# Performance work log

Hardware: AMD Instinct MI355X
Metric: run time of the kernel (lower is better)

Reference implementation:

```python
import jax, jax.numpy as jnp
import numpy as np

EPS = 1e-8  # matches torch.nn.functional.cosine_similarity default eps


def setup_inputs() -> dict:
    key = jax.random.key(0)
    k1, k2 = jax.random.split(key)
    B, C, L, D = 65536, 64, 64, 128
    x = jax.random.normal(k1, (B, D), dtype=jnp.float32)
    category_embeddings = jax.random.normal(k2, (C, L, D), dtype=jnp.float32)
    leaf_usage_counts = jnp.zeros((C, L), dtype=jnp.float32)
    return {
        "x": x,
        "category_embeddings": category_embeddings,
        "leaf_usage_counts": leaf_usage_counts,
    }


def reference(x, category_embeddings, leaf_usage_counts):
    # Cosine similarity: [B, C, L] without materializing the broadcast [B,C,L,D].
    x_norm = jnp.maximum(jnp.linalg.norm(x, axis=-1, keepdims=True), EPS)        # [B, 1]
    e_norm = jnp.maximum(jnp.linalg.norm(category_embeddings, axis=-1), EPS)     # [C, L]
    dots = jnp.einsum('bd,cld->bcl', x, category_embeddings)                     # [B, C, L]
    cosine_sim = dots / (x_norm[:, :, None] * e_norm[None, :, :])                # [B, C, L]

    # Training-path usage-count update (done under no_grad in torch):
    # per-category bincount of argmax leaf, scatter-added into the buffer.
    max_indices = jnp.argmax(cosine_sim, axis=2)                                 # [B, C] int
    C, L = leaf_usage_counts.shape
    cat_ids = jnp.broadcast_to(jnp.arange(C)[None, :], max_indices.shape)        # [B, C]
    leaf_counts = jnp.zeros((C, L), jnp.float32).at[cat_ids, max_indices].add(1.0)
    new_leaf_usage_counts = leaf_usage_counts + leaf_counts                      # [C, L]

    cosine_sim_max = jnp.max(cosine_sim, axis=2)                                 # [B, C]
    return cosine_sim_max, new_leaf_usage_counts
```

## Files before the change

kernel.cpp:

```cpp
#include <hip/hip_runtime.h>
#include <stdint.h>
#include <stddef.h>

#define D      128
#define NCATS  64
#define NLEAF  64
#define NC_BLK 8
#define BM     256
#define BIAS   32.0f

typedef _Float16 half8_t  __attribute__((ext_vector_type(8)));
typedef _Float16 half4h_t __attribute__((ext_vector_type(4)));
typedef float    float4_t __attribute__((ext_vector_type(4)));

__device__ __forceinline__ void async_ld16(const void* g, void* l) {
  __builtin_amdgcn_global_load_lds((const __attribute__((address_space(1))) uint32_t*)g,
                                   (__attribute__((address_space(3))) uint32_t*)l,
                                   16, 0, 0);
}

#define UMAX(a, b) ((a) > (b) ? (a) : (b))
#define DPP_REDUCE16(p)                                                                   \
  do {                                                                                    \
    unsigned _t;                                                                          \
    _t = (unsigned)__builtin_amdgcn_mov_dpp((int)(p), 0x121, 0xf, 0xf, false); p = UMAX(p, _t); \
    _t = (unsigned)__builtin_amdgcn_mov_dpp((int)(p), 0x122, 0xf, 0xf, false); p = UMAX(p, _t); \
    _t = (unsigned)__builtin_amdgcn_mov_dpp((int)(p), 0x124, 0xf, 0xf, false); p = UMAX(p, _t); \
    _t = (unsigned)__builtin_amdgcn_mov_dpp((int)(p), 0x128, 0xf, 0xf, false); p = UMAX(p, _t); \
  } while (0)

__global__ __launch_bounds__(256) void prep_e_kernel(const float* __restrict__ e,
                                                     char* __restrict__ e16,
                                                     const float* __restrict__ cin,
                                                     float* __restrict__ counts_out) {
  const int t  = threadIdx.x;
  const int rl = t >> 4;
  const int cc = t & 15;
  const int row = blockIdx.x * 16 + rl;
  const float* src = e + (size_t)row * D + cc * 8;
  float4_t v0 = *(const float4_t*)src;
  float4_t v1 = *(const float4_t*)(src + 4);
  float ss = v0.x*v0.x + v0.y*v0.y + v0.z*v0.z + v0.w*v0.w +
             v1.x*v1.x + v1.y*v1.y + v1.z*v1.z + v1.w*v1.w;
  ss += __shfl_xor(ss, 1);
  ss += __shfl_xor(ss, 2);
  ss += __shfl_xor(ss, 4);
  ss += __shfl_xor(ss, 8);
  const float inv = 1.0f / fmaxf(sqrtf(ss), 1e-8f);
  half8_t h;
  h[0] = (_Float16)(v0.x * inv); h[1] = (_Float16)(v0.y * inv);
  h[2] = (_Float16)(v0.z * inv); h[3] = (_Float16)(v0.w * inv);
  h[4] = (_Float16)(v1.x * inv); h[5] = (_Float16)(v1.y * inv);
  h[6] = (_Float16)(v1.z * inv); h[7] = (_Float16)(v1.w * inv);
  const int dc = cc ^ (rl & 7);
  *(half8_t*)(e16 + (size_t)row * 256 + dc * 16) = h;
  if (blockIdx.x < (NCATS * NLEAF) / 256)
    counts_out[blockIdx.x * 256 + t] = cin[blockIdx.x * 256 + t];
}

__global__ __launch_bounds__(256, 3) void main_kernel(const float* __restrict__ x,
                                                      const char* __restrict__ e16,
                                                      float* __restrict__ cos_out,
                                                      float* __restrict__ counts_out) {
  __shared__ __align__(16) char ebuf[2][16384];
  __shared__ unsigned hist[NC_BLK * NLEAF];
  __shared__ __align__(16) _Float16 stage[BM * 8];

  const int tid  = threadIdx.x;
  const int w    = tid >> 6;
  const int lane = tid & 63;
  const int q    = lane >> 4;
  const int wl   = lane & 15;

  const int rb     = blockIdx.x >> 3;
  const int c_base = (blockIdx.x & 7) * NC_BLK;
  const int b_base = rb * BM;

  for (int i = tid; i < NC_BLK * NLEAF; i += 256) hist[i] = 0;

  {
    const char* g = e16 + (size_t)c_base * 16384 + w * 4096 + lane * 16;
    char* l = &ebuf[0][w * 4096 + lane * 16];
#pragma unroll
    for (int j = 0; j < 4; ++j) async_ld16(g + j * 1024, l + j * 1024);
  }

  half8_t a[4][4];
  float inv_x[4];
#pragma unroll
  for (int rt = 0; rt < 4; ++rt) {
    const int row = b_base + w * 64 + rt * 16 + wl;
    const float* xr = x + (size_t)row * D;
    float ss = 0.f;
#pragma unroll
    for (int s = 0; s < 4; ++s) {
      const float* p = xr + s * 32 + q * 8;
      float4_t v0 = *(const float4_t*)p;
      float4_t v1 = *(const float4_t*)(p + 4);
      half8_t h;
      h[0] = (_Float16)v0.x; h[1] = (_Float16)v0.y;
      h[2] = (_Float16)v0.z; h[3] = (_Float16)v0.w;
      h[4] = (_Float16)v1.x; h[5] = (_Float16)v1.y;
      h[6] = (_Float16)v1.z; h[7] = (_Float16)v1.w;
      a[rt][s] = h;
      ss += v0.x*v0.x + v0.y*v0.y + v0.z*v0.z + v0.w*v0.w +
            v1.x*v1.x + v1.y*v1.y + v1.z*v1.z + v1.w*v1.w;
    }
    ss += __shfl_xor(ss, 16);
    ss += __shfl_xor(ss, 32);
    inv_x[rt] = 1.0f / fmaxf(sqrtf(ss), 1e-8f);
  }

  int rowbase[4], xoff[4];
#pragma unroll
  for (int nt = 0; nt < 4; ++nt) rowbase[nt] = (nt * 16 + wl) * 256;
#pragma unroll
  for (int s = 0; s < 4; ++s) xoff[s] = ((q + 4 * s) ^ (wl & 7)) * 16;

  const float4_t bias4 = {BIAS, BIAS, BIAS, BIAS};

  __syncthreads();

  for (int ci = 0; ci < NC_BLK; ++ci) {
    const char* cur = ebuf[ci & 1];

    if (ci + 1 < NC_BLK) {
      const char* g = e16 + (size_t)(c_base + ci + 1) * 16384 + w * 4096 + lane * 16;
      char* l = &ebuf[(ci + 1) & 1][w * 4096 + lane * 16];
#pragma unroll
      for (int j = 0; j < 4; ++j) async_ld16(g + j * 1024, l + j * 1024);
    }

    unsigned pk[4][4];
#pragma unroll
    for (int nt = 0; nt < 4; ++nt) {
      float4_t acc[4];
#pragma unroll
      for (int s = 0; s < 4; ++s) {
        half8_t b = *(const half8_t*)(cur + rowbase[nt] + xoff[s]);
#pragma unroll
        for (int rt = 0; rt < 4; ++rt)
          acc[rt] = __builtin_amdgcn_mfma_f32_16x16x32_f16(
              a[rt][s], b, (s == 0) ? bias4 : acc[rt], 0, 0, 0);
      }
      const unsigned idc = (unsigned)(nt * 16 + wl);
#pragma unroll
      for (int rt = 0; rt < 4; ++rt)
#pragma unroll
        for (int reg = 0; reg < 4; ++reg) {
          unsigned k = (__float_as_uint(acc[rt][reg]) & 0xFFFFFFC0u) | idc;
          pk[rt][reg] = (nt == 0) ? k : UMAX(pk[rt][reg], k);
        }
    }

#pragma unroll
    for (int rt = 0; rt < 4; ++rt)
#pragma unroll
      for (int reg = 0; reg < 4; ++reg) DPP_REDUCE16(pk[rt][reg]);

    if ((wl >> 2) == q) {
      const int reg = wl & 3;
#pragma unroll
      for (int rt = 0; rt < 4; ++rt) {
        const unsigned p = pk[rt][reg];
        const float val = (__uint_as_float(p & 0xFFFFFFC0u) - BIAS) * inv_x[rt];
        stage[(w * 64 + rt * 16 + wl) * 8 + ci] = (_Float16)val;
        atomicAdd(&hist[ci * NLEAF + (int)(p & 63u)], 1u);
      }
    }
    __syncthreads();
  }

  __syncthreads();

#pragma unroll
  for (int k = 0; k < 2; ++k) {
    const int id = k * 256 + tid;
    const int r  = id >> 1;
    const int c0 = (id & 1) * 4;
    half4h_t h = *(const half4h_t*)&stage[r * 8 + c0];
    float4_t v;
    v.x = (float)h[0]; v.y = (float)h[1]; v.z = (float)h[2]; v.w = (float)h[3];
    *(float4_t*)&cos_out[(size_t)(b_base + r) * NCATS + c_base + c0] = v;
  }

  for (int i = tid; i < NC_BLK * NLEAF; i += 256) {
    const unsigned v = hist[i];
    if (v) atomicAdd(&counts_out[c_base * NLEAF + i], (float)v);
  }
}

extern "C" void kernel_launch(void* const* d_in, const int* in_sizes, int n_in,
                              void* d_out, int out_size, void* d_ws, size_t ws_size,
                              hipStream_t stream) {
  const float* x   = (const float*)d_in[0];
  const float* e   = (const float*)d_in[1];
  const float* cin = (const float*)d_in[2];

  const int B = in_sizes[0] / D;
  const int erows = in_sizes[1] / D;
  float* cos_out = (float*)d_out;
  float* counts_out = cos_out + (size_t)B * NCATS;
  char* e16 = (char*)d_ws;

  prep_e_kernel<<<erows / 16, 256, 0, stream>>>(e, e16, cin, counts_out);
  main_kernel<<<(B / BM) * (NCATS / NC_BLK), 256, 0, stream>>>(x, e16, cos_out, counts_out);
}
```

Before: 162.3 us.

## Swap MFMA operand roles so leaves map to rows and argmax reduces in-lane

```diff
diff --git a/kernel.cpp b/kernel.cpp
--- a/kernel.cpp
+++ b/kernel.cpp
@@ -18,16 +18,6 @@
                                    (__attribute__((address_space(3))) uint32_t*)l,
                                    16, 0, 0);
 }
-
-#define UMAX(a, b) ((a) > (b) ? (a) : (b))
-#define DPP_REDUCE16(p)                                                                   \
-  do {                                                                                    \
-    unsigned _t;                                                                          \
-    _t = (unsigned)__builtin_amdgcn_mov_dpp((int)(p), 0x121, 0xf, 0xf, false); p = UMAX(p, _t); \
-    _t = (unsigned)__builtin_amdgcn_mov_dpp((int)(p), 0x122, 0xf, 0xf, false); p = UMAX(p, _t); \
-    _t = (unsigned)__builtin_amdgcn_mov_dpp((int)(p), 0x124, 0xf, 0xf, false); p = UMAX(p, _t); \
-    _t = (unsigned)__builtin_amdgcn_mov_dpp((int)(p), 0x128, 0xf, 0xf, false); p = UMAX(p, _t); \
-  } while (0)
 
 __global__ __launch_bounds__(256) void prep_e_kernel(const float* __restrict__ e,
                                                      char* __restrict__ e16,
@@ -85,11 +75,11 @@
     for (int j = 0; j < 4; ++j) async_ld16(g + j * 1024, l + j * 1024);
   }
 
-  half8_t a[4][4];
+  half8_t bfrag[4][4];
   float inv_x[4];
 #pragma unroll
-  for (int rt = 0; rt < 4; ++rt) {
-    const int row = b_base + w * 64 + rt * 16 + wl;
+  for (int nt = 0; nt < 4; ++nt) {
+    const int row = b_base + w * 64 + nt * 16 + wl;
     const float* xr = x + (size_t)row * D;
     float ss = 0.f;
 #pragma unroll
@@ -102,21 +92,22 @@
       h[2] = (_Float16)v0.z; h[3] = (_Float16)v0.w;
       h[4] = (_Float16)v1.x; h[5] = (_Float16)v1.y;
       h[6] = (_Float16)v1.z; h[7] = (_Float16)v1.w;
-      a[rt][s] = h;
+      bfrag[nt][s] = h;
       ss += v0.x*v0.x + v0.y*v0.y + v0.z*v0.z + v0.w*v0.w +
             v1.x*v1.x + v1.y*v1.y + v1.z*v1.z + v1.w*v1.w;
     }
     ss += __shfl_xor(ss, 16);
     ss += __shfl_xor(ss, 32);
-    inv_x[rt] = 1.0f / fmaxf(sqrtf(ss), 1e-8f);
+    inv_x[nt] = 1.0f / fmaxf(sqrtf(ss), 1e-8f);
   }
 
   int rowbase[4], xoff[4];
 #pragma unroll
-  for (int nt = 0; nt < 4; ++nt) rowbase[nt] = (nt * 16 + wl) * 256;
+  for (int rt = 0; rt < 4; ++rt) rowbase[rt] = (rt * 16 + wl) * 256;
 #pragma unroll
   for (int s = 0; s < 4; ++s) xoff[s] = ((q + 4 * s) ^ (wl & 7)) * 16;
 
+  const unsigned idq = (unsigned)(q << 2);
   const float4_t bias4 = {BIAS, BIAS, BIAS, BIAS};
 
   __syncthreads();
@@ -131,40 +122,45 @@
       for (int j = 0; j < 4; ++j) async_ld16(g + j * 1024, l + j * 1024);
     }
 
-    unsigned pk[4][4];
+    unsigned pk[4];
+#pragma unroll
+    for (int rt = 0; rt < 4; ++rt) {
+      float4_t acc[4];
+#pragma unroll
+      for (int s = 0; s < 4; ++s) {
+        half8_t ef = *(const half8_t*)(cur + rowbase[rt] + xoff[s]);
+#pragma unroll
+        for (int nt = 0; nt < 4; ++nt)
+          acc[nt] = __builtin_amdgcn_mfma_f32_16x16x32_f16(
+              ef, bfrag[nt][s], (s == 0) ? bias4 : acc[nt], 0, 0, 0);
+      }
+#pragma unroll
+      for (int nt = 0; nt < 4; ++nt)
+#pragma unroll
+        for (int reg = 0; reg < 4; ++reg) {
+          unsigned k = (__float_as_uint(acc[nt][reg]) & 0xFFFFFFC0u) |
+                       (unsigned)(rt * 16 + reg);
+          if (rt == 0 && reg == 0) pk[nt] = k;
+          else                     pk[nt] = (pk[nt] > k) ? pk[nt] : k;
+        }
+    }
+
 #pragma unroll
     for (int nt = 0; nt < 4; ++nt) {
-      float4_t acc[4];
-#pragma unroll
-      for (int s = 0; s < 4; ++s) {
-        half8_t b = *(const half8_t*)(cur + rowbase[nt] + xoff[s]);
-#pragma unroll
-        for (int rt = 0; rt < 4; ++rt)
-          acc[rt] = __builtin_amdgcn_mfma_f32_16x16x32_f16(
-              a[rt][s], b, (s == 0) ? bias4 : acc[rt], 0, 0, 0);
-      }
-      const unsigned idc = (unsigned)(nt * 16 + wl);
-#pragma unroll
-      for (int rt = 0; rt < 4; ++rt)
-#pragma unroll
-        for (int reg = 0; reg < 4; ++reg) {
-          unsigned k = (__float_as_uint(acc[rt][reg]) & 0xFFFFFFC0u) | idc;
-          pk[rt][reg] = (nt == 0) ? k : UMAX(pk[rt][reg], k);
-        }
-    }
-
-#pragma unroll
-    for (int rt = 0; rt < 4; ++rt)
-#pragma unroll
-      for (int reg = 0; reg < 4; ++reg) DPP_REDUCE16(pk[rt][reg]);
-
-    if ((wl >> 2) == q) {
-      const int reg = wl & 3;
-#pragma unroll
-      for (int rt = 0; rt < 4; ++rt) {
-        const unsigned p = pk[rt][reg];
-        const float val = (__uint_as_float(p & 0xFFFFFFC0u) - BIAS) * inv_x[rt];
-        stage[(w * 64 + rt * 16 + wl) * 8 + ci] = (_Float16)val;
+      unsigned v = pk[nt] | idq;
+      unsigned t = (unsigned)__shfl_xor((int)v, 16);
+      v = (v > t) ? v : t;
+      t = (unsigned)__shfl_xor((int)v, 32);
+      v = (v > t) ? v : t;
+      pk[nt] = v;
+    }
+
+    if (lane < 16) {
+#pragma unroll
+      for (int nt = 0; nt < 4; ++nt) {
+        const unsigned p = pk[nt];
+        const float val = (__uint_as_float(p & 0xFFFFFFC0u) - BIAS) * inv_x[nt];
+        stage[(w * 64 + nt * 16 + lane) * 8 + ci] = (_Float16)val;
         atomicAdd(&hist[ci * NLEAF + (int)(p & 63u)], 1u);
       }
     }
```

New measurement: 155.3 us. 4.3% less time.
